# Kernel optimization log

Measured on AMD Instinct MI355X. Metric: run time of the kernel, lower is better.

The kernel has to match this reference:

```python
import jax, jax.numpy as jnp
import numpy as np

B, T, C, L = 1024, 256, 100, 64  # batch, time steps, classes (blank=C-1), label length
NEG = -1e30   # safe -inf for log-space DP
EPS = 1e-7    # Keras K.epsilon() added before log


def setup_inputs() -> dict:
    key = jax.random.key(0)
    k1, k2 = jax.random.split(key)
    logits = jax.random.normal(k1, (B, T, C), dtype=jnp.float32)
    y_pred = jax.nn.softmax(logits, axis=-1)  # ctc_batch_cost expects probabilities
    y_true = jax.random.randint(k2, (B, L), 0, C - 1)  # labels in [0, C-2]; blank=C-1
    return {"y_true": y_true, "y_pred": y_pred}


def ctc_loss(y_true, y_pred):
    """Faithful K.ctc_batch_cost with full input/label lengths, blank = C-1."""
    Bb, Tt, Cc = y_pred.shape
    Ll = y_true.shape[1]
    S = 2 * Ll + 1  # extended label lattice: blank-interleaved
    blank = Cc - 1

    # extended labels: [blank, l0, blank, l1, ..., blank]
    ext = jnp.full((Bb, S), blank, dtype=y_true.dtype).at[:, 1::2].set(y_true)
    # skip-transition allowed when ext[s] is non-blank and differs from ext[s-2]
    ext_m2 = jnp.concatenate([jnp.full((Bb, 2), -1, ext.dtype), ext[:, :-2]], axis=1)
    allow = (ext != blank) & (ext != ext_m2)  # [B,S]

    logp = jnp.log(y_pred + EPS)  # [B,T,C]
    # gather log-probs on the lattice once: [B,T,S]
    lp_ext = jnp.take_along_axis(
        logp, jnp.broadcast_to(ext[:, None, :], (Bb, Tt, S)), axis=2)
    lp_seq = jnp.moveaxis(lp_ext, 1, 0)  # [T,B,S] for scan

    # alpha init: only states 0 (blank) and 1 (first label) reachable at t=0
    alpha0 = jnp.where(jnp.arange(S)[None, :] < 2, lp_seq[0], NEG)

    def shift(a, k):
        return jnp.concatenate(
            [jnp.full((Bb, k), NEG, a.dtype), a[:, :-k]], axis=1)

    def step(alpha, lp_t):
        new = jnp.logaddexp(
            jnp.logaddexp(alpha, shift(alpha, 1)),
            jnp.where(allow, shift(alpha, 2), NEG)) + lp_t
        return new, None

    alphaT, _ = jax.lax.scan(step, alpha0, lp_seq[1:])
    # total prob = alpha[T-1, S-1] + alpha[T-1, S-2]
    loss = -jnp.logaddexp(alphaT[:, -1], alphaT[:, -2])
    return loss[:, None]  # ctc_batch_cost returns shape [B,1]


def reference(y_true, y_pred):
    return ctc_loss(y_true, y_pred)
```

## Files before the change

### kernel.cpp

```cpp
#include <hip/hip_runtime.h>

#define B_ 1024
#define T_ 256
#define C_ 100
#define L_ 64
#define EPS_ 1e-7f
#define LN2 0.69314718055994530942f

#define CH 8
#define NCH 16
#define DEPTH 6

#define LOG2F(x) __builtin_amdgcn_logf(x)

typedef const __attribute__((address_space(1))) void GV;
typedef __attribute__((address_space(3))) void LV;

__device__ __forceinline__ void gload_lds4(const void* g, void* l) {
    __builtin_amdgcn_global_load_lds((GV*)g, (LV*)l, 4, 0, 0);
}

__device__ __forceinline__ float dpp_shr1(float x) {
    return __int_as_float(__builtin_amdgcn_update_dpp(
        0, __float_as_int(x), 0x138, 0xf, 0xf, false));
}
__device__ __forceinline__ float dpp_shl1(float x) {
    return __int_as_float(__builtin_amdgcn_update_dpp(
        0, __float_as_int(x), 0x130, 0xf, 0xf, false));
}

#define PLAN(x0_, x1_, x2_) do {                                          \
    float m_ = fmaxf(fmaxf(x0_, x1_), x2_);                               \
    _Pragma("unroll")                                                     \
    for (int d_ = 1; d_ < 64; d_ <<= 1) m_ = fmaxf(m_, __shfl_xor(m_, d_)); \
    const int e_ = (__float_as_int(m_) >> 23) & 255;                      \
    rs_K = 127 - e_;                                                      \
    rs_scale = __int_as_float((254 - e_) << 23);           \
} while (0)

#define APPLY(x0_, x1_, x2_) do { x0_ *= rs_scale; x1_ *= rs_scale;       \
    x2_ *= rs_scale; Sacc += rs_K; } while (0)

#define FSTEP(pb_, pl_) do {                                              \
    const float up1 = dpp_shr1(a1);                                       \
    const float s   = allow ? up1 : 0.0f;                                 \
    const float n0  = (a0 + up1) * (pb_);                                 \
    const float n1  = ((a1 + a0) + s) * (pl_);                            \
    const float n2  = (a2 + a1) * (pb_);                                  \
    a0 = n0; a1 = n1; a2 = n2;                                            \
} while (0)

#define BSTEP(pb_, pl_) do {                                              \
    const float db0 = dpp_shl1(a0);                                       \
    const float db1 = dpp_shl1(a1);                                       \
    const float sc0 = is63 ? a2 : db0;                                    \
    const float sk  = allowN ? db1 : 0.0f;    \
    const float n0  = (a0 + a1) * (pb_);                                  \
    const float n1  = ((a1 + sc0) + sk) * (pl_);                          \
    const float n2  = a2 * (pb_);                                         \
    a0 = n0; a1 = n1; a2 = n2;                                            \
} while (0)

#define WAIT_CHUNK(c_) do {                                               \
    const int n_ = 9 * ((NCH - 1 - (c_)) < (DEPTH - 1) ? (NCH - 1 - (c_)) \
                                                       : (DEPTH - 1));    \
    switch (n_) {                                                         \
    case 45: asm volatile("s_waitcnt vmcnt(45)" ::: "memory"); break;     \
    case 36: asm volatile("s_waitcnt vmcnt(36)" ::: "memory"); break;     \
    case 27: asm volatile("s_waitcnt vmcnt(27)" ::: "memory"); break;     \
    case 18: asm volatile("s_waitcnt vmcnt(18)" ::: "memory"); break;     \
    case  9: asm volatile("s_waitcnt vmcnt(9)"  ::: "memory"); break;     \
    default: asm volatile("s_waitcnt vmcnt(0)"  ::: "memory"); break;     \
    }                                                                     \
} while (0)

#define ISSUE(wv_, c_, toff_expr, boff_expr) do {                         \
    _Pragma("unroll")                                                     \
    for (int j_ = 0; j_ < CH; ++j_)                                       \
        gload_lds4(pL + (toff_expr) * C_, &plbuf[wv_][(c_) & 7][j_][0]);  \
    gload_lds4(pBlane + (boff_expr) * C_, &pbbuf[wv_][(c_) & 7][0]);      \
} while (0)

__global__ __launch_bounds__(128) void ctc_kernel(
    const int* __restrict__ y_true,
    const float* __restrict__ y_pred,
    float* __restrict__ out)
{
    __shared__ float plbuf[2][8][CH][64];
    __shared__ float pbbuf[2][8][64];
    __shared__ float sG0[64], sG1[64];
    __shared__ float sG2;
    __shared__ int   sSaccB;

    const int tid  = threadIdx.x;
    const int lane = tid & 63;
    const int wv   = tid >> 6;
    const int b    = blockIdx.x;

    const float* __restrict__ base = y_pred + (size_t)b * T_ * C_;
    const int  label   = y_true[b * L_ + lane];
    const int  labprev = __shfl_up(label, 1);
    const bool allow   = (lane == 0) || (label != labprev);
    const bool is63    = (lane == 63);
    const bool allowN  = (bool)__shfl_down((int)allow, 1);

    const float* __restrict__ pL = base + label;

    float a0 = 0.0f, a1 = 0.0f, a2 = 0.0f;
    float rs_scale = 1.0f;
    int   rs_K = 0, Sacc = 0;

    if (wv == 0) {
        const float* __restrict__ pBlane = base + (C_ - 1) + (lane & 7) * C_;
        #pragma unroll
        for (int c = 0; c < DEPTH; ++c) ISSUE(0, c, c * CH + j_, c * CH);

        #pragma unroll
        for (int c = 0; c < NCH; ++c) {
            WAIT_CHUNK(c);
            const int bi = c & 7;
            if (c == 0) {
                a0 = (lane == 0) ? (pbbuf[0][0][0] + EPS_) : 0.0f;
                a1 = (lane == 0) ? (plbuf[0][0][0][lane] + EPS_) : 0.0f;
                a2 = 0.0f;
                PLAN(a0, a1, a2);
                #pragma unroll
                for (int j = 1; j < CH; ++j)
                    FSTEP(pbbuf[0][bi][j] + EPS_, plbuf[0][bi][j][lane] + EPS_);
            } else {
                APPLY(a0, a1, a2);
                PLAN(a0, a1, a2);
                #pragma unroll
                for (int j = 0; j < CH; ++j)
                    FSTEP(pbbuf[0][bi][j] + EPS_, plbuf[0][bi][j][lane] + EPS_);
            }
            if (c + DEPTH < NCH) ISSUE(0, c + DEPTH, (c + DEPTH) * CH + j_, (c + DEPTH) * CH);
        }

        APPLY(a0, a1, a2);
        PLAN(a0, a1, a2);
        APPLY(a0, a1, a2);
    } else {
        const float* __restrict__ pBlane = base + (C_ - 1) + (T_ - 1 - (lane & 7)) * C_;
        #pragma unroll
        for (int c = 0; c < DEPTH; ++c) ISSUE(1, c, T_ - 1 - (c * CH + j_), -(c * CH));

        #pragma unroll
        for (int c = 0; c < NCH; ++c) {
            WAIT_CHUNK(c);
            const int bi = c & 7;
            if (c == 0) {
                a2 = pbbuf[1][0][0] + EPS_;
                a1 = is63 ? (plbuf[1][0][0][lane] + EPS_) : 0.0f;
                a0 = 0.0f;
                PLAN(a0, a1, a2);
                #pragma unroll
                for (int j = 1; j < CH; ++j)
                    BSTEP(pbbuf[1][bi][j] + EPS_, plbuf[1][bi][j][lane] + EPS_);
            } else {
                APPLY(a0, a1, a2);
                PLAN(a0, a1, a2);
                #pragma unroll
                for (int j = 0; j < CH; ++j)
                    BSTEP(pbbuf[1][bi][j] + EPS_, plbuf[1][bi][j][lane] + EPS_);
            }
            if (c + DEPTH < NCH) ISSUE(1, c + DEPTH, T_ - 1 - ((c + DEPTH) * CH + j_), -((c + DEPTH) * CH));
        }

        APPLY(a0, a1, a2);
        PLAN(a0, a1, a2);
        APPLY(a0, a1, a2);

        const float db0 = dpp_shl1(a0);
        const float db1 = dpp_shl1(a1);
        sG0[lane] = a0 + a1;
        sG1[lane] = a1 + (is63 ? a2 : db0) + (allowN ? db1 : 0.0f);
        if (is63) { sG2 = a2; sSaccB = Sacc; }
    }

    __syncthreads();

    if (wv == 0) {
        float prod = a0 * sG0[lane] + a1 * sG1[lane];
        if (is63) prod += a2 * sG2;
        #pragma unroll
        for (int d = 1; d < 64; d <<= 1) prod += __shfl_xor(prod, d);
        if (lane == 0)
            out[b] = -LN2 * (LOG2F(prod) - (float)(Sacc + sSaccB));
    }
}

extern "C" void kernel_launch(void* const* d_in, const int* in_sizes, int n_in,
                              void* d_out, int out_size, void* d_ws, size_t ws_size,
                              hipStream_t stream) {
    const int*   y_true = (const int*)d_in[0];
    const float* y_pred = (const float*)d_in[1];
    float*       out    = (float*)d_out;

    ctc_kernel<<<dim3(B_), dim3(128), 0, stream>>>(y_true, y_pred, out);
}
```

Baseline: 24.51 us.

## Stream full contiguous time-slabs into LDS with 16-byte async loads

Each wave now copies whole contiguous 8-timestep slabs of y_pred (3200 bytes per chunk) into an LDS ring using 16-byte global_load_lds transfers, replacing the per-label 4-byte gathers and separate blank loads. The label and blank probabilities are then read from LDS by class index. This cuts the number of load instructions, from 9 scattered loads per chunk to 4 wide coalesced ones, at the cost of moving the full 100-class row rather than only the needed entries. Prefetch depth drops from 6 to 3 with a 4-slot ring, and the vmcnt waits are adjusted to match.

```diff
diff --git a/kernel.cpp b/kernel.cpp
--- a/kernel.cpp
+++ b/kernel.cpp
@@ -9,15 +9,16 @@
 
 #define CH 8
 #define NCH 16
-#define DEPTH 6
+#define DEPTH 3
+#define BROW (T_ * C_ * 4)
 
 #define LOG2F(x) __builtin_amdgcn_logf(x)
 
 typedef const __attribute__((address_space(1))) void GV;
 typedef __attribute__((address_space(3))) void LV;
 
-__device__ __forceinline__ void gload_lds4(const void* g, void* l) {
-    __builtin_amdgcn_global_load_lds((GV*)g, (LV*)l, 4, 0, 0);
+__device__ __forceinline__ void gload_lds16(const void* g, void* l) {
+    __builtin_amdgcn_global_load_lds((GV*)g, (LV*)l, 16, 0, 0);
 }
 
 __device__ __forceinline__ float dpp_shr1(float x) {
@@ -54,31 +55,26 @@
     const float db0 = dpp_shl1(a0);                                       \
     const float db1 = dpp_shl1(a1);                                       \
     const float sc0 = is63 ? a2 : db0;                                    \
-    const float sk  = allowN ? db1 : 0.0f;    \
+    const float sk  = allowN ? db1 : 0.0f;                                \
     const float n0  = (a0 + a1) * (pb_);                                  \
     const float n1  = ((a1 + sc0) + sk) * (pl_);                          \
     const float n2  = a2 * (pb_);                                         \
     a0 = n0; a1 = n1; a2 = n2;                                            \
 } while (0)
 
-#define WAIT_CHUNK(c_) do {                                               \
-    const int n_ = 9 * ((NCH - 1 - (c_)) < (DEPTH - 1) ? (NCH - 1 - (c_)) \
-                                                       : (DEPTH - 1));    \
-    switch (n_) {                                                         \
-    case 45: asm volatile("s_waitcnt vmcnt(45)" ::: "memory"); break;     \
-    case 36: asm volatile("s_waitcnt vmcnt(36)" ::: "memory"); break;     \
-    case 27: asm volatile("s_waitcnt vmcnt(27)" ::: "memory"); break;     \
-    case 18: asm volatile("s_waitcnt vmcnt(18)" ::: "memory"); break;     \
-    case  9: asm volatile("s_waitcnt vmcnt(9)"  ::: "memory"); break;     \
-    default: asm volatile("s_waitcnt vmcnt(0)"  ::: "memory"); break;     \
-    }                                                                     \
+#define WAITC(c_) do {                                                    \
+    if ((c_) <= NCH - 3)      asm volatile("s_waitcnt vmcnt(8)" ::: "memory"); \
+    else if ((c_) == NCH - 2) asm volatile("s_waitcnt vmcnt(4)" ::: "memory"); \
+    else                      asm volatile("s_waitcnt vmcnt(0)" ::: "memory"); \
 } while (0)
 
-#define ISSUE(wv_, c_, toff_expr, boff_expr) do {                         \
+#define SISSUE(wv_, c_, off0_) do {                                       \
     _Pragma("unroll")                                                     \
-    for (int j_ = 0; j_ < CH; ++j_)                                       \
-        gload_lds4(pL + (toff_expr) * C_, &plbuf[wv_][(c_) & 7][j_][0]);  \
-    gload_lds4(pBlane + (boff_expr) * C_, &pbbuf[wv_][(c_) & 7][0]);      \
+    for (int k_ = 0; k_ < 4; ++k_) {                                      \
+        unsigned o_ = (unsigned)(off0_) + k_ * 1024u + ((unsigned)lane << 4); \
+        o_ = o_ < (BROW - 16u) ? o_ : (BROW - 16u);                       \
+        gload_lds16(bb + o_, &ring[wv_][(c_) & 3][k_ * 256]);             \
+    }                                                                     \
 } while (0)
 
 __global__ __launch_bounds__(128) void ctc_kernel(
@@ -86,8 +82,7 @@
     const float* __restrict__ y_pred,
     float* __restrict__ out)
 {
-    __shared__ float plbuf[2][8][CH][64];
-    __shared__ float pbbuf[2][8][64];
+    __shared__ float ring[2][4][1024];
     __shared__ float sG0[64], sG1[64];
     __shared__ float sG2;
     __shared__ int   sSaccB;
@@ -98,73 +93,70 @@
     const int b    = blockIdx.x;
 
     const float* __restrict__ base = y_pred + (size_t)b * T_ * C_;
+    const char*  __restrict__ bb   = (const char*)base;
     const int  label   = y_true[b * L_ + lane];
     const int  labprev = __shfl_up(label, 1);
     const bool allow   = (lane == 0) || (label != labprev);
     const bool is63    = (lane == 63);
     const bool allowN  = (bool)__shfl_down((int)allow, 1);
 
-    const float* __restrict__ pL = base + label;
-
     float a0 = 0.0f, a1 = 0.0f, a2 = 0.0f;
     float rs_scale = 1.0f;
     int   rs_K = 0, Sacc = 0;
 
     if (wv == 0) {
-        const float* __restrict__ pBlane = base + (C_ - 1) + (lane & 7) * C_;
         #pragma unroll
-        for (int c = 0; c < DEPTH; ++c) ISSUE(0, c, c * CH + j_, c * CH);
+        for (int c = 0; c < DEPTH; ++c) SISSUE(0, c, c * 3200);
 
         #pragma unroll
         for (int c = 0; c < NCH; ++c) {
-            WAIT_CHUNK(c);
-            const int bi = c & 7;
+            WAITC(c);
+            const float* __restrict__ sl = ring[0][c & 3];
             if (c == 0) {
-                a0 = (lane == 0) ? (pbbuf[0][0][0] + EPS_) : 0.0f;
-                a1 = (lane == 0) ? (plbuf[0][0][0][lane] + EPS_) : 0.0f;
+                a0 = (lane == 0) ? (sl[99] + EPS_) : 0.0f;
+                a1 = (lane == 0) ? (sl[label] + EPS_) : 0.0f;
                 a2 = 0.0f;
                 PLAN(a0, a1, a2);
                 #pragma unroll
                 for (int j = 1; j < CH; ++j)
-                    FSTEP(pbbuf[0][bi][j] + EPS_, plbuf[0][bi][j][lane] + EPS_);
+                    FSTEP(sl[j * 100 + 99] + EPS_, sl[j * 100 + label] + EPS_);
             } else {
                 APPLY(a0, a1, a2);
                 PLAN(a0, a1, a2);
                 #pragma unroll
                 for (int j = 0; j < CH; ++j)
-                    FSTEP(pbbuf[0][bi][j] + EPS_, plbuf[0][bi][j][lane] + EPS_);
+                    FSTEP(sl[j * 100 + 99] + EPS_, sl[j * 100 + label] + EPS_);
             }
-            if (c + DEPTH < NCH) ISSUE(0, c + DEPTH, (c + DEPTH) * CH + j_, (c + DEPTH) * CH);
+            if (c + DEPTH < NCH) SISSUE(0, c + DEPTH, (c + DEPTH) * 3200);
         }
 
         APPLY(a0, a1, a2);
         PLAN(a0, a1, a2);
         APPLY(a0, a1, a2);
     } else {
-        const float* __restrict__ pBlane = base + (C_ - 1) + (T_ - 1 - (lane & 7)) * C_;
         #pragma unroll
-        for (int c = 0; c < DEPTH; ++c) ISSUE(1, c, T_ - 1 - (c * CH + j_), -(c * CH));
+        for (int c = 0; c < DEPTH; ++c) SISSUE(1, c, 99200 - c * 3200);
 
         #pragma unroll
         for (int c = 0; c < NCH; ++c) {
-            WAIT_CHUNK(c);
-            const int bi = c & 7;
+            WAITC(c);
+            const float* __restrict__ sl = ring[1][c & 3];
             if (c == 0) {
-                a2 = pbbuf[1][0][0] + EPS_;
-                a1 = is63 ? (plbuf[1][0][0][lane] + EPS_) : 0.0f;
+                a2 = sl[799] + EPS_;
+                a1 = is63 ? (sl[700 + label] + EPS_) : 0.0f;
                 a0 = 0.0f;
                 PLAN(a0, a1, a2);
                 #pragma unroll
                 for (int j = 1; j < CH; ++j)
-                    BSTEP(pbbuf[1][bi][j] + EPS_, plbuf[1][bi][j][lane] + EPS_);
+                    BSTEP(sl[(7 - j) * 100 + 99] + EPS_, sl[(7 - j) * 100 + label] + EPS_);
             } else {
                 APPLY(a0, a1, a2);
                 PLAN(a0, a1, a2);
                 #pragma unroll
                 for (int j = 0; j < CH; ++j)
-                    BSTEP(pbbuf[1][bi][j] + EPS_, plbuf[1][bi][j][lane] + EPS_);
+                    BSTEP(sl[(7 - j) * 100 + 99] + EPS_, sl[(7 - j) * 100 + label] + EPS_);
             }
-            if (c + DEPTH < NCH) ISSUE(1, c + DEPTH, T_ - 1 - ((c + DEPTH) * CH + j_), -((c + DEPTH) * CH));
+            if (c + DEPTH < NCH) SISSUE(1, c + DEPTH, 99200 - (c + DEPTH) * 3200);
         }
 
         APPLY(a0, a1, a2);
```

Result: faster. 23.57 us (-3.9%).
